# Optimization experiments

Hardware: AMD Instinct MI355X
Metric: run time of the kernel (lower is better)

## Reference

```python
import jax, jax.numpy as jnp
import numpy as np

N_NODES = 100000
N_EDGES = 1600000
IN_DIM = 768
HIDDEN = 256
N_CLASSES = 3


def setup_inputs() -> dict:
    key = jax.random.key(0)
    k0, k1, k2, k3 = jax.random.split(key, 4)
    x = jax.random.normal(k0, (N_NODES, IN_DIM), dtype=jnp.float32)
    edge_index = jax.random.randint(k1, (2, N_EDGES), 0, N_NODES, dtype=jnp.int32)
    # Glorot-ish init for weights
    W1 = jax.random.normal(k2, (IN_DIM, HIDDEN), dtype=jnp.float32) * (1.0 / np.sqrt(IN_DIM))
    b1 = jnp.zeros((HIDDEN,), dtype=jnp.float32)
    W2 = jax.random.normal(k3, (HIDDEN, N_CLASSES), dtype=jnp.float32) * (1.0 / np.sqrt(HIDDEN))
    b2 = jnp.zeros((N_CLASSES,), dtype=jnp.float32)
    return {"x": x, "edge_index": edge_index, "W1": W1, "b1": b1, "W2": W2, "b2": b2}


def reference(x, edge_index, W1, b1, W2, b2):
    """dumb_GNN forward: GCNConv(768->H) -> relu -> (dropout=eval identity) -> Linear -> log_softmax.

    GCNConv math (PyG default): out = D^{-1/2} (A + I) D^{-1/2} X W + b
    """
    n = x.shape[0]
    src, dst = edge_index[0], edge_index[1]
    # add self-loops
    loops = jnp.arange(n, dtype=src.dtype)
    src = jnp.concatenate([src, loops])
    dst = jnp.concatenate([dst, loops])
    # symmetric degree normalization (degrees include self-loops)
    deg = jax.ops.segment_sum(jnp.ones_like(src, dtype=x.dtype), dst, num_segments=n)
    dinv = jnp.where(deg > 0, jax.lax.rsqrt(deg), jnp.zeros_like(deg))
    norm = dinv[src] * dinv[dst]  # [E+N]
    # transform then gather-scale-scatter aggregate
    h = x @ W1  # [N, H]
    agg = jax.ops.segment_sum(h[src] * norm[:, None], dst, num_segments=n) + b1
    h = jax.nn.relu(agg)
    # dropout is identity at inference
    logits = h @ W2 + b2  # [N, C]
    return jax.nn.log_softmax(logits, axis=-1)
```

## Files before the change

### kernel.cpp

```cpp
#include <hip/hip_runtime.h>
#include <hip/hip_bf16.h>
#include <math.h>

#define N_NODES 100000
#define N_EDGES 1600000
#define IN_DIM  768
#define HIDDEN  256

#define SCAN_B  256
#define N_SBLK  ((N_NODES + SCAN_B - 1) / SCAN_B)

#define H_OFF    0ull
#define ADJ_OFF  51200000ull
#define RS_OFF   57600000ull
#define CUR_OFF  58000016ull
#define DEG_OFF  58400016ull
#define DINV_OFF 58800016ull
#define W1T_OFF  59200016ull
#define BSUM_OFF 59593232ull

typedef short          bf16x8 __attribute__((ext_vector_type(8)));
typedef float          fp32x4 __attribute__((ext_vector_type(4)));
typedef unsigned short u16x4  __attribute__((ext_vector_type(4)));

__device__ inline short f2bf(float f) {
    union { float f; unsigned u; } c; c.f = f;
    unsigned u = c.u;
    unsigned r = u + 0x7FFFu + ((u >> 16) & 1u);
    return (short)(r >> 16);
}

__device__ inline fp32x4 bf4_to_f4(u16x4 v) {
    fp32x4 r;
    for (int j = 0; j < 4; j++) {
        union { unsigned u; float f; } c;
        c.u = ((unsigned)v[j]) << 16;
        r[j] = c.f;
    }
    return r;
}

__device__ inline void async16(const void* g, void* l) {
    __builtin_amdgcn_global_load_lds(
        (const __attribute__((address_space(1))) unsigned int*)g,
        (__attribute__((address_space(3))) unsigned int*)l,
        16, 0, 0);
}

__global__ void init_kernel(int* __restrict__ deg, int* __restrict__ cursor) {
    int i = blockIdx.x * blockDim.x + threadIdx.x;
    if (i < N_NODES) { deg[i] = 0; cursor[i] = 0; }
}

__global__ void w1t_kernel(const float* __restrict__ w1, short* __restrict__ w1t) {
    int i = blockIdx.x * blockDim.x + threadIdx.x;
    if (i < HIDDEN * IN_DIM) {
        int n = i / IN_DIM, k = i % IN_DIM;
        w1t[i] = f2bf(w1[(size_t)k * HIDDEN + n]);
    }
}

__global__ void count_kernel(const int* __restrict__ dst, int* __restrict__ deg) {
    int e = blockIdx.x * blockDim.x + threadIdx.x;
    if (e < N_EDGES) atomicAdd(&deg[dst[e]], 1);
}

__global__ __launch_bounds__(SCAN_B) void scan1_kernel(const int* __restrict__ deg,
                                                       int* __restrict__ bsum) {
    int i = blockIdx.x * SCAN_B + threadIdx.x;
    int v = (i < N_NODES) ? deg[i] : 0;
    for (int off = 32; off > 0; off >>= 1) v += __shfl_down(v, off, 64);
    __shared__ int wsum[SCAN_B / 64];
    int lane = threadIdx.x & 63, w = threadIdx.x >> 6;
    if (lane == 0) wsum[w] = v;
    __syncthreads();
    if (threadIdx.x == 0) {
        int s = 0;
        for (int j = 0; j < SCAN_B / 64; j++) s += wsum[j];
        bsum[blockIdx.x] = s;
    }
}

__global__ __launch_bounds__(512) void scan2_kernel(int* __restrict__ bsum) {
    __shared__ int s[512];
    int tid = threadIdx.x;
    int v = (tid < N_SBLK) ? bsum[tid] : 0;
    s[tid] = v;
    __syncthreads();
    for (int off = 1; off < 512; off <<= 1) {
        int t = (tid >= off) ? s[tid - off] : 0;
        __syncthreads();
        s[tid] += t;
        __syncthreads();
    }
    if (tid < N_SBLK) bsum[tid] = s[tid] - v;
}

__global__ __launch_bounds__(SCAN_B) void scan3_kernel(const int* __restrict__ deg,
                                                       const int* __restrict__ bsum,
                                                       int* __restrict__ row_start,
                                                       float* __restrict__ dinv) {
    __shared__ int s[SCAN_B];
    int i = blockIdx.x * SCAN_B + threadIdx.x;
    int tid = threadIdx.x;
    int d = (i < N_NODES) ? deg[i] : 0;
    s[tid] = d;
    __syncthreads();
    for (int off = 1; off < SCAN_B; off <<= 1) {
        int t = (tid >= off) ? s[tid - off] : 0;
        __syncthreads();
        s[tid] += t;
        __syncthreads();
    }
    if (i < N_NODES) {
        row_start[i] = bsum[blockIdx.x] + s[tid] - d;
        dinv[i] = rsqrtf((float)(d + 1));
        if (i == N_NODES - 1) row_start[N_NODES] = N_EDGES;
    }
}

__global__ void fill_kernel(const int* __restrict__ src, const int* __restrict__ dst,
                            const int* __restrict__ row_start, int* __restrict__ cursor,
                            int* __restrict__ adj) {
    int e = blockIdx.x * blockDim.x + threadIdx.x;
    if (e < N_EDGES) {
        int d = dst[e];
        int p = row_start[d] + atomicAdd(&cursor[d], 1);
        adj[p] = src[e];
    }
}

__global__ __launch_bounds__(512) void gemm1_kernel(const float* __restrict__ x,
                                                    const short* __restrict__ w1t,
                                                    const float* __restrict__ dinv,
                                                    unsigned short* __restrict__ h) {
    __shared__ __align__(16) short a_lds[2 * 128 * 32];
    __shared__ __align__(16) short b_lds[2 * 256 * 32];

    const int tid  = threadIdx.x;
    const int lane = tid & 63;
    const int wave = tid >> 6;
    const int wm = (wave >> 2) * 64;
    const int wn = (wave & 3) * 64;
    const int l15 = lane & 15;
    const int q   = lane >> 4;

    const int nwg = gridDim.x;
    const int xq = nwg >> 3, xr = nwg & 7;
    const int orig = blockIdx.x;
    const int xcd = orig & 7, idx = orig >> 3;
    const int wgid = (xcd < xr ? xcd * (xq + 1) : xr * (xq + 1) + (xcd - xr) * xq) + idx;
    const int row0 = wgid * 128;

    const int ar = tid >> 2;
    const int kq = tid & 3;
    int garow = row0 + ar;
    if (garow >= N_NODES) garow = N_NODES - 1;
    const float* axp = x + (size_t)garow * IN_DIM + kq * 8;
    const int asw  = (ar >> 1) & 3;
    const int aoff = ar * 32 + ((kq ^ asw) << 3);

    const short* bg[2];
    int blo[2];
#pragma unroll
    for (int i = 0; i < 2; i++) {
        int cd = (wave * 2 + i) * 64 + lane;
        int br = cd >> 2;
        int c  = cd & 3;
        bg[i]  = w1t + (size_t)br * IN_DIM + ((c ^ ((br >> 1) & 3)) * 8);
        blo[i] = cd * 16;
    }

    fp32x4 acc[4][4];
#pragma unroll
    for (int i = 0; i < 4; i++)
#pragma unroll
        for (int j = 0; j < 4; j++)
#pragma unroll
            for (int r = 0; r < 4; r++) acc[i][j][r] = 0.0f;

#define BSTAGE(buf, k0) do {                                                  \
        char* bb = (char*)(b_lds + (buf) * (256 * 32));                       \
        async16(bg[0] + (k0), bb + blo[0]);                                   \
        async16(bg[1] + (k0), bb + blo[1]);                                   \
    } while (0)

#define AWRITE(buf, v0, v1) do {                                              \
        short* ad = a_lds + (buf) * (128 * 32);                               \
        bf16x8 wv;                                                            \
        wv[0] = f2bf(v0[0]); wv[1] = f2bf(v0[1]);                             \
        wv[2] = f2bf(v0[2]); wv[3] = f2bf(v0[3]);                             \
        wv[4] = f2bf(v1[0]); wv[5] = f2bf(v1[1]);                             \
        wv[6] = f2bf(v1[2]); wv[7] = f2bf(v1[3]);                             \
        *(bf16x8*)(ad + aoff) = wv;                                           \
    } while (0)

    {
        fp32x4 na0 = *(const fp32x4*)(axp + 0);
        fp32x4 na1 = *(const fp32x4*)(axp + 4);
        BSTAGE(0, 0);
        AWRITE(0, na0, na1);
        __syncthreads();
    }

    const int fsw = q ^ ((l15 >> 1) & 3);

    int cur = 0;
    for (int t = 0; t < IN_DIM / 32; ++t) {
        const int kn = (t + 1) * 32;
        const bool more = kn < IN_DIM;
        fp32x4 na0, na1;
        if (more) {
            na0 = *(const fp32x4*)(axp + kn);
            na1 = *(const fp32x4*)(axp + kn + 4);
            BSTAGE(cur ^ 1, kn);
        }

        const short* ac = a_lds + cur * (128 * 32);
        const short* bc = b_lds + cur * (256 * 32);
        bf16x8 af[4], bfr[4];
#pragma unroll
        for (int mt = 0; mt < 4; mt++)
            af[mt] = *(const bf16x8*)(ac + (wm + mt * 16 + l15) * 32 + (fsw << 3));
#pragma unroll
        for (int nt = 0; nt < 4; nt++)
            bfr[nt] = *(const bf16x8*)(bc + (wn + nt * 16 + l15) * 32 + (fsw << 3));
#pragma unroll
        for (int mt = 0; mt < 4; mt++)
#pragma unroll
            for (int nt = 0; nt < 4; nt++)
                acc[mt][nt] = __builtin_amdgcn_mfma_f32_16x16x32_bf16(
                    af[mt], bfr[nt], acc[mt][nt], 0, 0, 0);

        if (more) AWRITE(cur ^ 1, na0, na1);

        __syncthreads();
        cur ^= 1;
    }
#undef BSTAGE
#undef AWRITE

    float dv[4][4];
#pragma unroll
    for (int mt = 0; mt < 4; mt++)
#pragma unroll
        for (int r = 0; r < 4; r++) {
            int row = row0 + wm + mt * 16 + q * 4 + r;
            dv[mt][r] = (row < N_NODES) ? dinv[row] : 0.0f;
        }
#pragma unroll
    for (int mt = 0; mt < 4; mt++) {
#pragma unroll
        for (int nt = 0; nt < 4; nt++) {
            int col = wn + nt * 16 + l15;
#pragma unroll
            for (int r = 0; r < 4; r++) {
                int row = row0 + wm + mt * 16 + q * 4 + r;
                if (row < N_NODES)
                    h[(size_t)row * HIDDEN + col] =
                        (unsigned short)f2bf(dv[mt][r] * acc[mt][nt][r]);
            }
        }
    }
}

__global__ __launch_bounds__(256) void aggregate_kernel(
    const unsigned short* __restrict__ h, const int* __restrict__ adj,
    const int* __restrict__ row_start, const float* __restrict__ dinv,
    const float* __restrict__ b1, const float* __restrict__ w2,
    const float* __restrict__ b2, float* __restrict__ out) {
    const int lane = threadIdx.x & 63;
    const int wave = threadIdx.x >> 6;
    const int v = blockIdx.x * 4 + wave;
    if (v >= N_NODES) return;

    const size_t loff = (size_t)lane * 4;

    fp32x4 a0 = bf4_to_f4(*(const u16x4*)(h + (size_t)v * HIDDEN + loff));
    fp32x4 a1 = {0,0,0,0}, a2 = {0,0,0,0}, a3 = {0,0,0,0};

    int e0 = row_start[v], e1 = row_start[v + 1];
    for (int e = e0; e < e1; e += 64) {
        int cnt = min(64, e1 - e);
        int s = (lane < cnt) ? adj[e + lane] : 0;
        int i = 0;
        for (; i + 4 <= cnt; i += 4) {
            int s0 = __shfl(s, i,     64);
            int s1 = __shfl(s, i + 1, 64);
            int s2 = __shfl(s, i + 2, 64);
            int s3 = __shfl(s, i + 3, 64);
            u16x4 r0 = *(const u16x4*)(h + (size_t)s0 * HIDDEN + loff);
            u16x4 r1 = *(const u16x4*)(h + (size_t)s1 * HIDDEN + loff);
            u16x4 r2 = *(const u16x4*)(h + (size_t)s2 * HIDDEN + loff);
            u16x4 r3 = *(const u16x4*)(h + (size_t)s3 * HIDDEN + loff);
            a0 += bf4_to_f4(r0);
            a1 += bf4_to_f4(r1);
            a2 += bf4_to_f4(r2);
            a3 += bf4_to_f4(r3);
        }
        for (; i < cnt; i++) {
            int si = __shfl(s, i, 64);
            a0 += bf4_to_f4(*(const u16x4*)(h + (size_t)si * HIDDEN + loff));
        }
    }
    fp32x4 acc = (a0 + a1) + (a2 + a3);

    float dvv = dinv[v];
    fp32x4 bb = *(const fp32x4*)(b1 + loff);
    float hr[4];
    for (int j = 0; j < 4; j++) hr[j] = fmaxf(0.0f, dvv * acc[j] + bb[j]);

    float p0 = 0.f, p1 = 0.f, p2 = 0.f;
    for (int j = 0; j < 4; j++) {
        const float* wr = w2 + (size_t)(lane * 4 + j) * 3;
        p0 += hr[j] * wr[0];
        p1 += hr[j] * wr[1];
        p2 += hr[j] * wr[2];
    }
    for (int off = 32; off > 0; off >>= 1) {
        p0 += __shfl_down(p0, off, 64);
        p1 += __shfl_down(p1, off, 64);
        p2 += __shfl_down(p2, off, 64);
    }
    if (lane == 0) {
        p0 += b2[0]; p1 += b2[1]; p2 += b2[2];
        float m = fmaxf(p0, fmaxf(p1, p2));
        float l = logf(expf(p0 - m) + expf(p1 - m) + expf(p2 - m));
        out[(size_t)v * 3 + 0] = p0 - m - l;
        out[(size_t)v * 3 + 1] = p1 - m - l;
        out[(size_t)v * 3 + 2] = p2 - m - l;
    }
}

extern "C" void kernel_launch(void* const* d_in, const int* in_sizes, int n_in,
                              void* d_out, int out_size, void* d_ws, size_t ws_size,
                              hipStream_t stream) {
    const float* x    = (const float*)d_in[0];
    const int*   ei   = (const int*)d_in[1];
    const float* W1   = (const float*)d_in[2];
    const float* b1   = (const float*)d_in[3];
    const float* W2   = (const float*)d_in[4];
    const float* b2   = (const float*)d_in[5];
    float* out = (float*)d_out;

    const int* src = ei;
    const int* dst = ei + N_EDGES;

    char* ws = (char*)d_ws;
    unsigned short* h_ws = (unsigned short*)(ws + H_OFF);
    int*   adj       = (int*)(ws + ADJ_OFF);
    int*   row_start = (int*)(ws + RS_OFF);
    int*   cursor    = (int*)(ws + CUR_OFF);
    int*   deg       = (int*)(ws + DEG_OFF);
    float* dinv      = (float*)(ws + DINV_OFF);
    short* w1t       = (short*)(ws + W1T_OFF);
    int*   bsum      = (int*)(ws + BSUM_OFF);

    init_kernel<<<(N_NODES + 255) / 256, 256, 0, stream>>>(deg, cursor);
    w1t_kernel<<<(HIDDEN * IN_DIM + 255) / 256, 256, 0, stream>>>(W1, w1t);
    count_kernel<<<(N_EDGES + 255) / 256, 256, 0, stream>>>(dst, deg);
    scan1_kernel<<<N_SBLK, SCAN_B, 0, stream>>>(deg, bsum);
    scan2_kernel<<<1, 512, 0, stream>>>(bsum);
    scan3_kernel<<<N_SBLK, SCAN_B, 0, stream>>>(deg, bsum, row_start, dinv);
    fill_kernel<<<(N_EDGES + 255) / 256, 256, 0, stream>>>(src, dst, row_start, cursor, adj);
    gemm1_kernel<<<(N_NODES + 127) / 128, 512, 0, stream>>>(x, w1t, dinv, h_ws);
    aggregate_kernel<<<N_NODES / 4, 256, 0, stream>>>(h_ws, adj, row_start, dinv, b1, W2, b2, out);
}
```

Baseline: 725.5 us.

## Triple-buffer B tiles in GEMM and use vector index loads in aggregation

The GEMM now keeps three LDS buffers for the W1 tile, issuing async loads two K-steps ahead. It replaces __syncthreads with a partial vmcnt wait plus barrier, so the next B stage can stay in flight across the barrier. The aggregation kernel drops the per-chunk cooperative adj load and shuffles, and instead has each lane read neighbor indices with aligned int4 loads, prefetching the next group. This removes shuffle overhead but makes every lane load the same index addresses (a broadcast), and it adds extra LDS use in the GEMM, which may lower occupancy.

Measured after the change: 747.7 us. +3.1%, slower.

```diff
diff --git a/kernel.cpp b/kernel.cpp
--- a/kernel.cpp
+++ b/kernel.cpp
@@ -135,7 +135,7 @@
                                                     const float* __restrict__ dinv,
                                                     unsigned short* __restrict__ h) {
     __shared__ __align__(16) short a_lds[2 * 128 * 32];
-    __shared__ __align__(16) short b_lds[2 * 256 * 32];
+    __shared__ __align__(16) short b_lds[3 * 256 * 32];
 
     const int tid  = threadIdx.x;
     const int lane = tid & 63;
@@ -144,6 +144,7 @@
     const int wn = (wave & 3) * 64;
     const int l15 = lane & 15;
     const int q   = lane >> 4;
+    const int NT  = IN_DIM / 32;
 
     const int nwg = gridDim.x;
     const int xq = nwg >> 3, xr = nwg & 7;
@@ -195,29 +196,38 @@
         *(bf16x8*)(ad + aoff) = wv;                                           \
     } while (0)
 
+#define KBAR() do {                                                           \
+        asm volatile("s_waitcnt vmcnt(2) lgkmcnt(0)" ::: "memory");           \
+        __builtin_amdgcn_s_barrier();                                         \
+    } while (0)
+
     {
-        fp32x4 na0 = *(const fp32x4*)(axp + 0);
-        fp32x4 na1 = *(const fp32x4*)(axp + 4);
+        fp32x4 p0 = *(const fp32x4*)(axp + 0);
+        fp32x4 p1 = *(const fp32x4*)(axp + 4);
         BSTAGE(0, 0);
-        AWRITE(0, na0, na1);
-        __syncthreads();
+        AWRITE(0, p0, p1);
+        BSTAGE(1, 32);
+        KBAR();
     }
 
     const int fsw = q ^ ((l15 >> 1) & 3);
 
     int cur = 0;
-    for (int t = 0; t < IN_DIM / 32; ++t) {
+    int bread = 0;
+    int btgt = 2;
+    for (int t = 0; t < NT; ++t) {
         const int kn = (t + 1) * 32;
-        const bool more = kn < IN_DIM;
+        const bool haveA = kn < IN_DIM;
         fp32x4 na0, na1;
-        if (more) {
+        if (haveA) {
             na0 = *(const fp32x4*)(axp + kn);
             na1 = *(const fp32x4*)(axp + kn + 4);
-            BSTAGE(cur ^ 1, kn);
         }
+        if (t + 2 < NT) BSTAGE(btgt, (t + 2) * 32);
+        __builtin_amdgcn_sched_barrier(0);
 
         const short* ac = a_lds + cur * (128 * 32);
-        const short* bc = b_lds + cur * (256 * 32);
+        const short* bc = b_lds + bread * (256 * 32);
         bf16x8 af[4], bfr[4];
 #pragma unroll
         for (int mt = 0; mt < 4; mt++)
@@ -232,13 +242,16 @@
                 acc[mt][nt] = __builtin_amdgcn_mfma_f32_16x16x32_bf16(
                     af[mt], bfr[nt], acc[mt][nt], 0, 0, 0);
 
-        if (more) AWRITE(cur ^ 1, na0, na1);
-
-        __syncthreads();
+        if (haveA) AWRITE(cur ^ 1, na0, na1);
+
+        KBAR();
         cur ^= 1;
+        bread = (bread == 2) ? 0 : bread + 1;
+        btgt  = (btgt  == 2) ? 0 : btgt  + 1;
     }
 #undef BSTAGE
 #undef AWRITE
+#undef KBAR
 
     float dv[4][4];
 #pragma unroll
@@ -279,29 +292,31 @@
     fp32x4 a0 = bf4_to_f4(*(const u16x4*)(h + (size_t)v * HIDDEN + loff));
     fp32x4 a1 = {0,0,0,0}, a2 = {0,0,0,0}, a3 = {0,0,0,0};
 
-    int e0 = row_start[v], e1 = row_start[v + 1];
-    for (int e = e0; e < e1; e += 64) {
-        int cnt = min(64, e1 - e);
-        int s = (lane < cnt) ? adj[e + lane] : 0;
-        int i = 0;
-        for (; i + 4 <= cnt; i += 4) {
-            int s0 = __shfl(s, i,     64);
-            int s1 = __shfl(s, i + 1, 64);
-            int s2 = __shfl(s, i + 2, 64);
-            int s3 = __shfl(s, i + 3, 64);
-            u16x4 r0 = *(const u16x4*)(h + (size_t)s0 * HIDDEN + loff);
-            u16x4 r1 = *(const u16x4*)(h + (size_t)s1 * HIDDEN + loff);
-            u16x4 r2 = *(const u16x4*)(h + (size_t)s2 * HIDDEN + loff);
-            u16x4 r3 = *(const u16x4*)(h + (size_t)s3 * HIDDEN + loff);
+    const int e0 = row_start[v], e1 = row_start[v + 1];
+    int e = e0;
+    while ((e & 3) && e < e1) {
+        int si = adj[e];
+        a0 += bf4_to_f4(*(const u16x4*)(h + (size_t)si * HIDDEN + loff));
+        ++e;
+    }
+    if (e + 4 <= e1) {
+        int4 ss = *(const int4*)(adj + e);
+        for (; e + 4 <= e1; e += 4) {
+            int4 nx = ss;
+            if (e + 8 <= e1) ss = *(const int4*)(adj + e + 4);
+            u16x4 r0 = *(const u16x4*)(h + (size_t)nx.x * HIDDEN + loff);
+            u16x4 r1 = *(const u16x4*)(h + (size_t)nx.y * HIDDEN + loff);
+            u16x4 r2 = *(const u16x4*)(h + (size_t)nx.z * HIDDEN + loff);
+            u16x4 r3 = *(const u16x4*)(h + (size_t)nx.w * HIDDEN + loff);
             a0 += bf4_to_f4(r0);
             a1 += bf4_to_f4(r1);
             a2 += bf4_to_f4(r2);
             a3 += bf4_to_f4(r3);
         }
-        for (; i < cnt; i++) {
-            int si = __shfl(s, i, 64);
-            a0 += bf4_to_f4(*(const u16x4*)(h + (size_t)si * HIDDEN + loff));
-        }
+    }
+    for (; e < e1; ++e) {
+        int si = adj[e];
+        a0 += bf4_to_f4(*(const u16x4*)(h + (size_t)si * HIDDEN + loff));
     }
     fp32x4 acc = (a0 + a1) + (a2 + a3);
 
```
